# Performance work log

Measured on AMD Instinct MI355X. Metric: run time of the kernel, lower is better.

## Reference

```python
import jax, jax.numpy as jnp
import numpy as np

N_NODES = 10000
N_EDGES = 160000
H = 4            # attention heads
HID = 128        # out_channels == gnn_hidden_dim
C = HID          # per-head channels after .view(-1, H, C) with C = out_channels
HC = H * C       # 512
QD, KD, VD = 19, 16, 18
OUT = 2
SCALE = (HID // H) ** -0.5  # (out_channels // heads) ** -0.5


def _segment_softmax(alpha, idx, n):
    # PyG-style softmax over edges grouped by destination node, per head.
    amax = jax.ops.segment_max(alpha, idx, num_segments=n)          # [n, H]
    ex = jnp.exp(alpha - amax[idx])                                  # [E, H]
    den = jax.ops.segment_sum(ex, idx, num_segments=n)               # [n, H]
    return ex / (den[idx] + 1e-16)


def _gat_layer(qf, kf, vf, pos, src, dst, wq, wk, wv, wo, bo):
    n = qf.shape[0]
    q = (qf @ wq).reshape(n, H, C)
    k = (kf @ wk).reshape(n, H, C)
    v = (vf @ wv).reshape(n, H, C)
    # position-decayed attention: exp(-||pos_i - pos_j||), c_decay = 1.0
    dist = jnp.linalg.norm(pos[dst] - pos[src], axis=-1)             # [E]
    pos_weight = jnp.exp(-dist)
    alpha = (q[dst] * k[src]).sum(-1) * SCALE * pos_weight[:, None]  # [E, H]
    alpha = _segment_softmax(alpha, dst, n)
    out = jax.ops.segment_sum(v[src] * alpha[..., None], dst, num_segments=n)  # [n, H, C]
    return out.reshape(n, HC) @ wo + bo                              # concat heads -> lin_out


def setup_inputs() -> dict:
    key = jax.random.key(0)
    ks = jax.random.split(key, 16)

    def w(k, shape):  # xavier-uniform-ish scale
        return jax.random.normal(k, shape, jnp.float32) * np.float32(np.sqrt(2.0 / (shape[0] + shape[1])))

    obs = jax.random.normal(ks[0], (N_NODES, 37), jnp.float32)
    edge_index = jax.random.randint(ks[1], (2, N_EDGES), 0, N_NODES, jnp.int32)
    return dict(
        obs=obs, edge_index=edge_index,
        wq0=w(ks[2], (QD, HC)), wk0=w(ks[3], (KD, HC)), wv0=w(ks[4], (VD, HC)),
        wo0=w(ks[5], (HC, HID)), bo0=jnp.zeros((HID,), jnp.float32),
        wq1=w(ks[6], (HID, HC)), wk1=w(ks[7], (HID, HC)), wv1=w(ks[8], (HID, HC)),
        wo1=w(ks[9], (HC, HID)), bo1=jnp.zeros((HID,), jnp.float32),
        w1=w(ks[10], (HID, 256)), b1=jnp.zeros((256,), jnp.float32),
        w2=w(ks[11], (256, 256)), b2=jnp.zeros((256,), jnp.float32),
        w3=w(ks[12], (256, OUT)), b3=jnp.zeros((OUT,), jnp.float32),
    )


def reference(obs, edge_index, wq0, wk0, wv0, wo0, bo0, wq1, wk1, wv1, wo1, bo1, w1, b1, w2, b2, w3, b3):
    pos = obs[:, :2]
    # query: agent-self slices 0:12 plus tail slices 30:37 -> 19 dims
    qf = jnp.concatenate([obs[:, :12], obs[:, 30:37]], axis=-1)
    # key: neighbor_block 12:24 + obstacle_block 26:30 -> 16 dims
    kf = jnp.concatenate([obs[:, 12:24], obs[:, 26:30]], axis=-1)
    # value: neighbor_block + neighbor_progress + obstacle_block = 12:30 -> 18 dims
    vf = obs[:, 12:30]
    src, dst = edge_index[0], edge_index[1]
    h = _gat_layer(qf, kf, vf, pos, src, dst, wq0, wk0, wv0, wo0, bo0)
    h = _gat_layer(h, h, h, pos, src, dst, wq1, wk1, wv1, wo1, bo1)
    h = jax.nn.relu(h @ w1 + b1)
    h = jax.nn.relu(h @ w2 + b2)
    return h @ w3 + b3
```

## Files before the change

### kernel.cpp

```cpp
#include <hip/hip_runtime.h>
#include <math.h>

#define NN 10000
#define NE 160000
#define CAP 64
#define SCALE_F 0.17677669529663687f
#define LOG2E_F 1.4426950408889634f

typedef _Float16 f16x8 __attribute__((ext_vector_type(8)));
typedef _Float16 f16x2 __attribute__((ext_vector_type(2)));
typedef float f32x4 __attribute__((ext_vector_type(4)));

#if defined(__has_builtin)
#if __has_builtin(__builtin_amdgcn_global_load_lds)
#define HAS_GLL 1
#endif
#if __has_builtin(__builtin_amdgcn_fdot2)
#define HAS_FDOT2 1
#endif
#endif

struct __align__(8) Edge { int s; float pw; };

__device__ __forceinline__ float dot8_f16(f16x8 a, f16x8 b, float acc) {
#ifdef HAS_FDOT2
#pragma unroll
  for (int e = 0; e < 4; ++e) {
    f16x2 aa = {a[2 * e], a[2 * e + 1]};
    f16x2 bb = {b[2 * e], b[2 * e + 1]};
    acc = __builtin_amdgcn_fdot2(aa, bb, acc, false);
  }
#else
#pragma unroll
  for (int e = 0; e < 8; ++e) acc += (float)a[e] * (float)b[e];
#endif
  return acc;
}

__global__ __launch_bounds__(256) void scatter_kernel(const int* __restrict__ src, const int* __restrict__ dst,
                                                      const float* __restrict__ obs, int* __restrict__ counts,
                                                      Edge* __restrict__ edges) {
  int e = blockIdx.x * 256 + threadIdx.x;
  if (e >= NE) return;
  int s = src[e], d = dst[e];
  int p = atomicAdd(&counts[d], 1);
  float dx = obs[d * 37 + 0] - obs[s * 37 + 0];
  float dy = obs[d * 37 + 1] - obs[s * 37 + 1];
  Edge ee;
  ee.s = s;
  ee.pw = SCALE_F * LOG2E_F * __expf(-sqrtf(dx * dx + dy * dy));
  edges[d * CAP + p] = ee;
}

__global__ __launch_bounds__(256) void prep_kernel(const float* __restrict__ wq0, const float* __restrict__ wk0,
                                                   const float* __restrict__ wv0,
                                                   const float* __restrict__ wo0, const float* __restrict__ wq1,
                                                   const float* __restrict__ wk1, const float* __restrict__ wv1,
                                                   const float* __restrict__ wo1, const float* __restrict__ w1,
                                                   const float* __restrict__ w2, _Float16* __restrict__ dst,
                                                   const float* __restrict__ obs, _Float16* __restrict__ A0,
                                                   int* __restrict__ counts, const float* __restrict__ b3,
                                                   float* __restrict__ outg) {
  int t = blockIdx.x * 256 + threadIdx.x;
  if (t >= 524288) {
    int tp = t - 524288;
    if (tp < NN * 64) {
      int n = tp >> 6, k = tp & 63;
      const float* o = obs + n * 37;
      float x = 0.f;
      if (k < 12) x = o[k];
      else if (k < 19) x = o[30 + k - 12];
      else if (k < 31) x = o[12 + k - 19];
      else if (k < 35) x = o[26 + k - 31];
      else if (k < 53) x = o[12 + k - 35];
      A0[tp] = (_Float16)x;
      return;
    }
    int tz = tp - NN * 64;
    if (tz < NN) { counts[tz] = 0; return; }
    int to = tz - NN;
    if (to < 2 * NN) outg[to] = b3[to & 1];
    return;
  }
  if (t < 98304) {
    int c = t >> 6, k = t & 63;
    float x = 0.f;
    if (c < 512) { if (k < 19) x = wq0[k * 512 + c]; }
    else if (c < 1024) { if (k >= 19 && k < 35) x = wk0[(k - 19) * 512 + (c - 512)]; }
    else { if (k >= 35 && k < 53) x = wv0[(k - 35) * 512 + (c - 1024)]; }
    dst[t] = (_Float16)x;
    return;
  }
  int t1 = t - 98304;
  if (t1 < 196608) {
    int c = t1 >> 7, k = t1 & 127;
    float x;
    if (c < 512) x = wq1[k * 512 + c];
    else if (c < 1024) x = wk1[k * 512 + (c - 512)];
    else x = wv1[k * 512 + (c - 1024)];
    dst[98304 + t1] = (_Float16)x;
    return;
  }
  int t2 = t1 - 196608;
  if (t2 < 65536) { int n = t2 >> 9, k = t2 & 511; dst[294912 + t2] = (_Float16)wo0[k * 128 + n]; return; }
  int t3 = t2 - 65536;
  if (t3 < 65536) { int n = t3 >> 9, k = t3 & 511; dst[360448 + t3] = (_Float16)wo1[k * 128 + n]; return; }
  int t4 = t3 - 65536;
  if (t4 < 32768) { int n = t4 >> 7, k = t4 & 127; dst[425984 + t4] = (_Float16)w1[k * 256 + n]; return; }
  int t5 = t4 - 32768;
  if (t5 < 65536) { int n = t5 >> 8, k = t5 & 255; dst[458752 + t5] = (_Float16)w2[k * 256 + n]; }
}

__global__ __launch_bounds__(256) void gat_kernel(const _Float16* __restrict__ qh, const _Float16* __restrict__ KV,
                                                  const int* __restrict__ counts, const Edge* __restrict__ edges,
                                                  _Float16* __restrict__ attH) {
  int wave = threadIdx.x >> 6, lane = threadIdx.x & 63;
  int grp = lane >> 4, l15 = lane & 15;
  int r = blockIdx.x & 7;
  int c = blockIdx.x >> 3;
  int head = r & 3;
  int chunk = c * 2 + (r >> 2);
  int n = chunk * 4 + wave;
  const _Float16* kvbase = KV + (size_t)head * NN * 256 + l15 * 8;
  f16x8 qv = *(const f16x8*)(qh + (size_t)head * NN * 128 + n * 128 + l15 * 8);
  int cnt = counts[n];
  const Edge* eb = edges + (size_t)n * CAP;
  float den = 0.f;
  float o[8] = {};
  for (int j = grp; j < cnt; j += 8) {
    int jB = j + 4;
    bool actB = jB < cnt;
    int iB = actB ? jB : j;
    Edge eA = eb[j];
    Edge eB = eb[iB];
    const _Float16* pA = kvbase + (size_t)eA.s * 256;
    const _Float16* pB = kvbase + (size_t)eB.s * 256;
    f16x8 kA = *(const f16x8*)pA;
    f16x8 kB = *(const f16x8*)pB;
    f16x8 vA = *(const f16x8*)(pA + 128);
    f16x8 vB = *(const f16x8*)(pB + 128);
    float dA = dot8_f16(qv, kA, 0.f);
    float dB = dot8_f16(qv, kB, 0.f);
    dA += __shfl_xor(dA, 1); dB += __shfl_xor(dB, 1);
    dA += __shfl_xor(dA, 2); dB += __shfl_xor(dB, 2);
    dA += __shfl_xor(dA, 4); dB += __shfl_xor(dB, 4);
    dA += __shfl_xor(dA, 8); dB += __shfl_xor(dB, 8);
    float wA = exp2f(fminf(dA * eA.pw, 80.f));
    float wB = actB ? exp2f(fminf(dB * eB.pw, 80.f)) : 0.f;
    den += wA + wB;
#pragma unroll
    for (int e = 0; e < 8; ++e)
      o[e] += wA * (float)vA[e] + wB * (float)vB[e];
  }
#pragma unroll
  for (int off = 16; off <= 32; off <<= 1) {
    den += __shfl_xor(den, off);
#pragma unroll
    for (int e = 0; e < 8; ++e) o[e] += __shfl_xor(o[e], off);
  }
  if (grp == 0) {
    float inv = 1.f / (den + 1e-16f);
    f16x8 rr;
#pragma unroll
    for (int e = 0; e < 8; ++e) rr[e] = (_Float16)(o[e] * inv);
    *(f16x8*)(attH + (size_t)head * NN * 128 + n * 128 + l15 * 8) = rr;
  }
}

template <int BM, int BIAS, int RELU, int SPLIT, int FUSE3, int SEGA, int PIN>
__global__ __launch_bounds__(256) void gemm_mfma(const _Float16* __restrict__ A, const _Float16* __restrict__ BT,
                                                 const float* __restrict__ bias, _Float16* __restrict__ C,
                                                 _Float16* __restrict__ KV, const float* __restrict__ w3g,
                                                 float* __restrict__ outg, int M, int N, int K) {
  constexpr int ACH = BM / 32;
  constexpr int WR = BM / 2;
  constexpr int RF = WR / 16;
  __shared__ _Float16 As[2][BM * 64];
  __shared__ _Float16 Bs[2][64 * 64];
  int tid = threadIdx.x;
  int wave = tid >> 6, lane = tid & 63;
  int l15 = lane & 15, lq = lane >> 4;
  int wr = (wave >> 1) * WR, wc = (wave & 1) * 32;
  int bx, by;
  if (PIN) {
    int xcd = blockIdx.x & 7, slot = blockIdx.x >> 3;
    int hh = xcd & 3, half = xcd >> 2;
    int i = half * 237 + slot;
    int bg = i / 79;
    bx = i - bg * 79;
    by = (bg < 2) ? (2 * hh + bg) : (bg < 4) ? (8 + 2 * hh + (bg - 2)) : (16 + 2 * hh + (bg - 4));
  } else {
    bx = blockIdx.x;
    by = blockIdx.y;
  }
  int m0 = bx * BM, n0 = by * 64;
  f32x4 acc[RF][2] = {};
  int sw = (l15 & 7) << 4;
  int nt = K >> 6;

  auto stage = [&](int buf, int k0) {
#pragma unroll
    for (int i = 0; i < ACH; ++i) {
      int P = (wave * ACH + i) * 1024 + lane * 16;
      int row = P >> 7;
      int cl = (P & 127) ^ ((row & 7) << 4);
      int gr = m0 + row;
      if (gr > M - 1) gr = M - 1;
      const _Float16* g;
      if (SEGA)
        g = A + (size_t)(k0 >> 7) * (NN * 128) + (size_t)gr * 128 + (k0 & 64) + (cl >> 1);
      else
        g = A + (size_t)gr * K + k0 + (cl >> 1);
#ifdef HAS_GLL
      __builtin_amdgcn_global_load_lds((const __attribute__((address_space(1))) void*)g,
                                       (__attribute__((address_space(3))) void*)((char*)As[buf] + (wave * ACH + i) * 1024),
                                       16, 0, 0);
#else
      uint4 tv = *(const uint4*)g;
      *(uint4*)((char*)As[buf] + P) = tv;
#endif
    }
#pragma unroll
    for (int i = 0; i < 2; ++i) {
      int P = (wave * 2 + i) * 1024 + lane * 16;
      int row = P >> 7;
      int cl = (P & 127) ^ ((row & 7) << 4);
      const _Float16* g = BT + (size_t)(n0 + row) * K + k0 + (cl >> 1);
#ifdef HAS_GLL
      __builtin_amdgcn_global_load_lds((const __attribute__((address_space(1))) void*)g,
                                       (__attribute__((address_space(3))) void*)((char*)Bs[buf] + (wave * 2 + i) * 1024),
                                       16, 0, 0);
#else
      uint4 tv = *(const uint4*)g;
      *(uint4*)((char*)Bs[buf] + P) = tv;
#endif
    }
  };

  stage(0, 0);
  __syncthreads();
  for (int t = 0; t < nt; ++t) {
    int cur = t & 1;
    if (t + 1 < nt) stage(cur ^ 1, (t + 1) << 6);
    const char* pa = (const char*)As[cur];
    const char* pb = (const char*)Bs[cur];
#pragma unroll
    for (int ks = 0; ks < 2; ++ks) {
      int cc = ((ks * 32 + lq * 8) << 1) ^ sw;
      f16x8 b0 = *(const f16x8*)(pb + (wc + 0 + l15) * 128 + cc);
      f16x8 b1 = *(const f16x8*)(pb + (wc + 16 + l15) * 128 + cc);
#pragma unroll
      for (int ri = 0; ri < RF; ++ri) {
        f16x8 a0 = *(const f16x8*)(pa + (wr + ri * 16 + l15) * 128 + cc);
        acc[ri][0] = __builtin_amdgcn_mfma_f32_16x16x32_f16(a0, b0, acc[ri][0], 0, 0, 0);
        acc[ri][1] = __builtin_amdgcn_mfma_f32_16x16x32_f16(a0, b1, acc[ri][1], 0, 0, 0);
      }
    }
    __syncthreads();
  }
#pragma unroll
  for (int ri = 0; ri < RF; ++ri) {
    int gr0 = m0 + wr + ri * 16 + lq * 4;
    float p0[4], p1[4];
#pragma unroll
    for (int jj = 0; jj < 4; ++jj) { p0[jj] = 0.f; p1[jj] = 0.f; }
#pragma unroll
    for (int ci = 0; ci < 2; ++ci) {
      int gc = n0 + wc + ci * 16 + l15;
      float bb = 0.f;
      if (BIAS) bb = bias[gc];
      float w30 = 0.f, w31 = 0.f;
      if (FUSE3) { w30 = w3g[gc * 2 + 0]; w31 = w3g[gc * 2 + 1]; }
#pragma unroll
      for (int jj = 0; jj < 4; ++jj) {
        int gr = gr0 + jj;
        float x = acc[ri][ci][jj] + bb;
        if (RELU) x = fmaxf(x, 0.f);
        if (FUSE3) {
          p0[jj] += x * w30;
          p1[jj] += x * w31;
        } else if (gr < M) {
          _Float16 val = (_Float16)x;
          if (SPLIT) {
            if (gc < 512) {
              int hh = gc >> 7, ch = gc & 127;
              C[((size_t)hh * NN + gr) * 128 + ch] = val;
            } else if (gc < 1024) {
              int hh = (gc - 512) >> 7, ch = (gc - 512) & 127;
              KV[((size_t)hh * NN + gr) * 256 + ch] = val;
            } else {
              int hh = (gc - 1024) >> 7, ch = (gc - 1024) & 127;
              KV[((size_t)hh * NN + gr) * 256 + 128 + ch] = val;
            }
          } else {
            C[(size_t)gr * N + gc] = val;
          }
        }
      }
    }
    if (FUSE3) {
#pragma unroll
      for (int jj = 0; jj < 4; ++jj) {
#pragma unroll
        for (int off = 1; off <= 8; off <<= 1) {
          p0[jj] += __shfl_xor(p0[jj], off);
          p1[jj] += __shfl_xor(p1[jj], off);
        }
        int gr = gr0 + jj;
        if (l15 == 0 && gr < M) {
          atomicAdd(&outg[gr * 2 + 0], p0[jj]);
          atomicAdd(&outg[gr * 2 + 1], p1[jj]);
        }
      }
    }
  }
}

extern "C" void kernel_launch(void* const* d_in, const int* in_sizes, int n_in,
                              void* d_out, int out_size, void* d_ws, size_t ws_size,
                              hipStream_t stream) {
  const float* obs = (const float*)d_in[0];
  const int* eidx = (const int*)d_in[1];
  const float* wq0 = (const float*)d_in[2];
  const float* wk0 = (const float*)d_in[3];
  const float* wv0 = (const float*)d_in[4];
  const float* wo0 = (const float*)d_in[5];
  const float* bo0 = (const float*)d_in[6];
  const float* wq1 = (const float*)d_in[7];
  const float* wk1 = (const float*)d_in[8];
  const float* wv1 = (const float*)d_in[9];
  const float* wo1 = (const float*)d_in[10];
  const float* bo1 = (const float*)d_in[11];
  const float* w1 = (const float*)d_in[12];
  const float* b1 = (const float*)d_in[13];
  const float* w2 = (const float*)d_in[14];
  const float* b2 = (const float*)d_in[15];
  const float* w3 = (const float*)d_in[16];
  const float* b3 = (const float*)d_in[17];
  float* outp = (float*)d_out;

  char* wsb = (char*)d_ws;
  _Float16* qh = (_Float16*)(wsb + 0);
  _Float16* KVB = (_Float16*)(wsb + 10240000);
  _Float16* attH = (_Float16*)(wsb + 30720000);
  _Float16* h = (_Float16*)(wsb + 40960000);
  _Float16* A0 = (_Float16*)(wsb + 43520000);
  _Float16* wT = (_Float16*)(wsb + 44800000);
  int* counts = (int*)(wsb + 45848576);
  Edge* edges = (Edge*)(wsb + 45888576);
  _Float16* m1 = attH;

  _Float16* w0T = wT + 0;
  _Float16* wqkv1T = wT + 98304;
  _Float16* wo0T = wT + 294912;
  _Float16* wo1T = wT + 360448;
  _Float16* w1T = wT + 425984;
  _Float16* w2T = wT + 458752;

  const int* e_src = eidx;
  const int* e_dst = eidx + NE;

  prep_kernel<<<4666, 256, 0, stream>>>(wq0, wk0, wv0, wo0, wq1, wk1, wv1, wo1, w1, w2, wT, obs, A0,
                                        counts, b3, outp);
  scatter_kernel<<<(NE + 255) / 256, 256, 0, stream>>>(e_src, e_dst, obs, counts, edges);

  gemm_mfma<128, 0, 0, 1, 0, 0, 1><<<1896, 256, 0, stream>>>(A0, w0T, nullptr, qh, KVB, nullptr, nullptr, NN, 1536, 64);
  gat_kernel<<<10000, 256, 0, stream>>>(qh, KVB, counts, edges, attH);
  gemm_mfma<32, 1, 0, 0, 0, 1, 0><<<dim3(313, 2), 256, 0, stream>>>(attH, wo0T, bo0, h, nullptr, nullptr, nullptr, NN, 128, 512);

  gemm_mfma<128, 0, 0, 1, 0, 0, 1><<<1896, 256, 0, stream>>>(h, wqkv1T, nullptr, qh, KVB, nullptr, nullptr, NN, 1536, 128);
  gat_kernel<<<10000, 256, 0, stream>>>(qh, KVB, counts, edges, attH);
  gemm_mfma<32, 1, 0, 0, 0, 1, 0><<<dim3(313, 2), 256, 0, stream>>>(attH, wo1T, bo1, h, nullptr, nullptr, nullptr, NN, 128, 512);

  gemm_mfma<64, 1, 1, 0, 0, 0, 0><<<dim3(157, 4), 256, 0, stream>>>(h, w1T, b1, m1, nullptr, nullptr, nullptr, NN, 256, 128);
  gemm_mfma<64, 1, 1, 0, 1, 0, 0><<<dim3(157, 4), 256, 0, stream>>>(m1, w2T, b2, nullptr, nullptr, w3, outp, NN, 256, 256);
}
```

Measured before the change: 148.8 us.

## Fuse the two MLP GEMMs and output projection into one kernel

Replaces the two separate MLP GEMM launches (w1 with relu, then w2 with relu plus the w3 projection) with a single kernel. Each block handles 32 rows and keeps the hidden activation m1 in LDS, streaming w2 tiles through shared memory. This drops the global round trip of m1 and one kernel launch. In exchange it launches only 313 blocks with large LDS use (72 KB), which lowers occupancy, and each block reloads the full w1 and w2 weights.

```diff
diff --git a/kernel.cpp b/kernel.cpp
--- a/kernel.cpp
+++ b/kernel.cpp
@@ -167,11 +167,10 @@
   }
 }
 
-template <int BM, int BIAS, int RELU, int SPLIT, int FUSE3, int SEGA, int PIN>
+template <int BM, int BIAS, int RELU, int SPLIT, int SEGA, int PIN>
 __global__ __launch_bounds__(256) void gemm_mfma(const _Float16* __restrict__ A, const _Float16* __restrict__ BT,
                                                  const float* __restrict__ bias, _Float16* __restrict__ C,
-                                                 _Float16* __restrict__ KV, const float* __restrict__ w3g,
-                                                 float* __restrict__ outg, int M, int N, int K) {
+                                                 _Float16* __restrict__ KV, int M, int N, int K) {
   constexpr int ACH = BM / 32;
   constexpr int WR = BM / 2;
   constexpr int RF = WR / 16;
@@ -261,25 +260,17 @@
 #pragma unroll
   for (int ri = 0; ri < RF; ++ri) {
     int gr0 = m0 + wr + ri * 16 + lq * 4;
-    float p0[4], p1[4];
-#pragma unroll
-    for (int jj = 0; jj < 4; ++jj) { p0[jj] = 0.f; p1[jj] = 0.f; }
 #pragma unroll
     for (int ci = 0; ci < 2; ++ci) {
       int gc = n0 + wc + ci * 16 + l15;
       float bb = 0.f;
       if (BIAS) bb = bias[gc];
-      float w30 = 0.f, w31 = 0.f;
-      if (FUSE3) { w30 = w3g[gc * 2 + 0]; w31 = w3g[gc * 2 + 1]; }
 #pragma unroll
       for (int jj = 0; jj < 4; ++jj) {
         int gr = gr0 + jj;
         float x = acc[ri][ci][jj] + bb;
         if (RELU) x = fmaxf(x, 0.f);
-        if (FUSE3) {
-          p0[jj] += x * w30;
-          p1[jj] += x * w31;
-        } else if (gr < M) {
+        if (gr < M) {
           _Float16 val = (_Float16)x;
           if (SPLIT) {
             if (gc < 512) {
@@ -298,19 +289,157 @@
         }
       }
     }
-    if (FUSE3) {
-#pragma unroll
-      for (int jj = 0; jj < 4; ++jj) {
-#pragma unroll
-        for (int off = 1; off <= 8; off <<= 1) {
-          p0[jj] += __shfl_xor(p0[jj], off);
-          p1[jj] += __shfl_xor(p1[jj], off);
-        }
-        int gr = gr0 + jj;
-        if (l15 == 0 && gr < M) {
-          atomicAdd(&outg[gr * 2 + 0], p0[jj]);
-          atomicAdd(&outg[gr * 2 + 1], p1[jj]);
-        }
+  }
+}
+
+__global__ __launch_bounds__(256) void mlp_kernel(const _Float16* __restrict__ h, const _Float16* __restrict__ w1T,
+                                                  const float* __restrict__ b1, const _Float16* __restrict__ w2T,
+                                                  const float* __restrict__ b2, const float* __restrict__ w3,
+                                                  float* __restrict__ outg) {
+  __shared__ __align__(16) char lds[73728];
+  const int LDS_H = 0, LDS_W1 = 8192, LDS_M1 = 0, LDS_W2 = 16384;
+  int tid = threadIdx.x;
+  int wave = tid >> 6, lane = tid & 63;
+  int l15 = lane & 15, lq = lane >> 4;
+  int m0 = blockIdx.x * 32;
+  int wn = wave * 64;
+
+#pragma unroll
+  for (int i = 0; i < 2; ++i) {
+    int P = (wave * 2 + i) * 1024 + lane * 16;
+    int row = P >> 8;
+    int cl = (P & 255) ^ ((row & 15) << 4);
+    int gr = m0 + row;
+    if (gr > NN - 1) gr = NN - 1;
+    const _Float16* g = h + (size_t)gr * 128 + (cl >> 1);
+#ifdef HAS_GLL
+    __builtin_amdgcn_global_load_lds((const __attribute__((address_space(1))) void*)g,
+                                     (__attribute__((address_space(3))) void*)(lds + LDS_H + (wave * 2 + i) * 1024),
+                                     16, 0, 0);
+#else
+    *(uint4*)(lds + LDS_H + P) = *(const uint4*)g;
+#endif
+  }
+#pragma unroll
+  for (int i = 0; i < 16; ++i) {
+    int P = (wave * 16 + i) * 1024 + lane * 16;
+    int row = P >> 8;
+    int cl = (P & 255) ^ ((row & 15) << 4);
+    const _Float16* g = w1T + (size_t)row * 128 + (cl >> 1);
+#ifdef HAS_GLL
+    __builtin_amdgcn_global_load_lds((const __attribute__((address_space(1))) void*)g,
+                                     (__attribute__((address_space(3))) void*)(lds + LDS_W1 + (wave * 16 + i) * 1024),
+                                     16, 0, 0);
+#else
+    *(uint4*)(lds + LDS_W1 + P) = *(const uint4*)g;
+#endif
+  }
+  __syncthreads();
+
+  f32x4 acc1[2][4] = {};
+#pragma unroll
+  for (int ks = 0; ks < 4; ++ks) {
+    int kcb = (ks * 32 + lq * 8) << 1;
+    f16x8 bfr[4];
+#pragma unroll
+    for (int ci = 0; ci < 4; ++ci) {
+      int brow = wn + ci * 16 + l15;
+      bfr[ci] = *(const f16x8*)(lds + LDS_W1 + brow * 256 + (kcb ^ ((brow & 15) << 4)));
+    }
+#pragma unroll
+    for (int ri = 0; ri < 2; ++ri) {
+      int arow = ri * 16 + l15;
+      f16x8 a = *(const f16x8*)(lds + LDS_H + arow * 256 + (kcb ^ ((arow & 15) << 4)));
+#pragma unroll
+      for (int ci = 0; ci < 4; ++ci)
+        acc1[ri][ci] = __builtin_amdgcn_mfma_f32_16x16x32_f16(a, bfr[ci], acc1[ri][ci], 0, 0, 0);
+    }
+  }
+  __syncthreads();
+#pragma unroll
+  for (int ri = 0; ri < 2; ++ri) {
+#pragma unroll
+    for (int ci = 0; ci < 4; ++ci) {
+      int ncol = wn + ci * 16 + l15;
+      float bb = b1[ncol];
+#pragma unroll
+      for (int j = 0; j < 4; ++j) {
+        int mrow = ri * 16 + lq * 4 + j;
+        float x = fmaxf(acc1[ri][ci][j] + bb, 0.f);
+        *(_Float16*)(lds + LDS_M1 + mrow * 512 + ((ncol * 2) ^ ((mrow & 15) << 4))) = (_Float16)x;
+      }
+    }
+  }
+  __syncthreads();
+
+  f32x4 acc2[2][4] = {};
+  for (int ks = 0; ks < 4; ++ks) {
+#pragma unroll
+    for (int i = 0; i < 8; ++i) {
+      int P = (wave * 8 + i) * 1024 + lane * 16;
+      int row = P >> 7;
+      int cl = (P & 127) ^ ((row & 7) << 4);
+      const _Float16* g = w2T + (size_t)row * 256 + ks * 64 + (cl >> 1);
+#ifdef HAS_GLL
+      __builtin_amdgcn_global_load_lds((const __attribute__((address_space(1))) void*)g,
+                                       (__attribute__((address_space(3))) void*)(lds + LDS_W2 + (wave * 8 + i) * 1024),
+                                       16, 0, 0);
+#else
+      *(uint4*)(lds + LDS_W2 + P) = *(const uint4*)g;
+#endif
+    }
+    __syncthreads();
+#pragma unroll
+    for (int kk = 0; kk < 2; ++kk) {
+      int kglob = (ks * 64 + kk * 32 + lq * 8) << 1;
+      int kcb2 = (kk * 32 + lq * 8) << 1;
+      f16x8 bfr[4];
+#pragma unroll
+      for (int ci = 0; ci < 4; ++ci) {
+        int brow = wn + ci * 16 + l15;
+        bfr[ci] = *(const f16x8*)(lds + LDS_W2 + brow * 128 + (kcb2 ^ ((brow & 7) << 4)));
+      }
+#pragma unroll
+      for (int ri = 0; ri < 2; ++ri) {
+        int arow = ri * 16 + l15;
+        f16x8 a = *(const f16x8*)(lds + LDS_M1 + arow * 512 + (kglob ^ ((arow & 15) << 4)));
+#pragma unroll
+        for (int ci = 0; ci < 4; ++ci)
+          acc2[ri][ci] = __builtin_amdgcn_mfma_f32_16x16x32_f16(a, bfr[ci], acc2[ri][ci], 0, 0, 0);
+      }
+    }
+    __syncthreads();
+  }
+
+  float p0[2][4] = {}, p1[2][4] = {};
+#pragma unroll
+  for (int ri = 0; ri < 2; ++ri) {
+#pragma unroll
+    for (int ci = 0; ci < 4; ++ci) {
+      int ncol = wn + ci * 16 + l15;
+      float bb = b2[ncol];
+      float w30 = w3[ncol * 2 + 0], w31 = w3[ncol * 2 + 1];
+#pragma unroll
+      for (int j = 0; j < 4; ++j) {
+        float x = fmaxf(acc2[ri][ci][j] + bb, 0.f);
+        p0[ri][j] += x * w30;
+        p1[ri][j] += x * w31;
+      }
+    }
+  }
+#pragma unroll
+  for (int ri = 0; ri < 2; ++ri) {
+#pragma unroll
+    for (int j = 0; j < 4; ++j) {
+#pragma unroll
+      for (int off = 1; off <= 8; off <<= 1) {
+        p0[ri][j] += __shfl_xor(p0[ri][j], off);
+        p1[ri][j] += __shfl_xor(p1[ri][j], off);
+      }
+      int gr = m0 + ri * 16 + lq * 4 + j;
+      if (l15 == 0 && gr < NN) {
+        atomicAdd(&outg[gr * 2 + 0], p0[ri][j]);
+        atomicAdd(&outg[gr * 2 + 1], p1[ri][j]);
       }
     }
   }
@@ -348,7 +477,6 @@
   _Float16* wT = (_Float16*)(wsb + 44800000);
   int* counts = (int*)(wsb + 45848576);
   Edge* edges = (Edge*)(wsb + 45888576);
-  _Float16* m1 = attH;
 
   _Float16* w0T = wT + 0;
   _Float16* wqkv1T = wT + 98304;
@@ -364,14 +492,13 @@
                                         counts, b3, outp);
   scatter_kernel<<<(NE + 255) / 256, 256, 0, stream>>>(e_src, e_dst, obs, counts, edges);
 
-  gemm_mfma<128, 0, 0, 1, 0, 0, 1><<<1896, 256, 0, stream>>>(A0, w0T, nullptr, qh, KVB, nullptr, nullptr, NN, 1536, 64);
+  gemm_mfma<128, 0, 0, 1, 0, 1><<<1896, 256, 0, stream>>>(A0, w0T, nullptr, qh, KVB, NN, 1536, 64);
   gat_kernel<<<10000, 256, 0, stream>>>(qh, KVB, counts, edges, attH);
-  gemm_mfma<32, 1, 0, 0, 0, 1, 0><<<dim3(313, 2), 256, 0, stream>>>(attH, wo0T, bo0, h, nullptr, nullptr, nullptr, NN, 128, 512);
-
-  gemm_mfma<128, 0, 0, 1, 0, 0, 1><<<1896, 256, 0, stream>>>(h, wqkv1T, nullptr, qh, KVB, nullptr, nullptr, NN, 1536, 128);
+  gemm_mfma<32, 1, 0, 0, 1, 0><<<dim3(313, 2), 256, 0, stream>>>(attH, wo0T, bo0, h, nullptr, NN, 128, 512);
+
+  gemm_mfma<128, 0, 0, 1, 0, 1><<<1896, 256, 0, stream>>>(h, wqkv1T, nullptr, qh, KVB, NN, 1536, 128);
   gat_kernel<<<10000, 256, 0, stream>>>(qh, KVB, counts, edges, attH);
-  gemm_mfma<32, 1, 0, 0, 0, 1, 0><<<dim3(313, 2), 256, 0, stream>>>(attH, wo1T, bo1, h, nullptr, nullptr, nullptr, NN, 128, 512);
-
-  gemm_mfma<64, 1, 1, 0, 0, 0, 0><<<dim3(157, 4), 256, 0, stream>>>(h, w1T, b1, m1, nullptr, nullptr, nullptr, NN, 256, 128);
-  gemm_mfma<64, 1, 1, 0, 1, 0, 0><<<dim3(157, 4), 256, 0, stream>>>(m1, w2T, b2, nullptr, nullptr, w3, outp, NN, 256, 256);
-}
+  gemm_mfma<32, 1, 0, 0, 1, 0><<<dim3(313, 2), 256, 0, stream>>>(attH, wo1T, bo1, h, nullptr, NN, 128, 512);
+
+  mlp_kernel<<<313, 256, 0, stream>>>(h, w1T, b1, w2T, b2, w3, outp);
+}
```

After: 140.6 us (median of 2 runs). 5.5% less time.
